# Optimization experiments

Hardware: AMD Instinct MI355X
Metric: run time of the kernel (lower is better)

Reference implementation:

```python
import jax, jax.numpy as jnp
import numpy as np

K = 9            # connections per output pixel
GA = 2           # global additional samples
RA = 2           # relative additional samples
VS = 4 + GA + RA # 2^rank neighbours + sampled
REGION = 12      # int(0.25 * 48) per spatial dim
MMULT = 0.1
MIN_SIGMA = 0.05
SIGMA_SCALE = 0.05
SIGMA_BOOST = 2.0


def setup_inputs() -> dict:
    key = jax.random.key(0)
    ks = jax.random.split(key, 8)
    b, cin, h, w = 8, 128, 48, 48
    cout = 256
    hidden = cin * 4

    def lin_init(k, fan_out, fan_in):
        bound = 1.0 / np.sqrt(fan_in)
        kw, kb = jax.random.split(k)
        W = jax.random.uniform(kw, (fan_out, fan_in), minval=-bound, maxval=bound, dtype=jnp.float32)
        bb = jax.random.uniform(kb, (fan_out,), minval=-bound, maxval=bound, dtype=jnp.float32)
        return W, bb

    x = jax.random.normal(ks[0], (b, cin, h, w), dtype=jnp.float32)
    W1, b1 = lin_init(ks[1], hidden, 2)          # toparams layer 1 (adaptive=False -> 2 coord inputs)
    W2, b2 = lin_init(ks[2], 3 * K, hidden)      # toparams layer 2 -> k means (2d) + k sigmas
    Wu, bu = lin_init(ks[3], cout, K * cin)      # unify linear
    gints = jax.random.randint(ks[4], (b, h, w, K, GA, 2), 0, h, dtype=jnp.int32)      # global samples (h==w)
    roff = jax.random.randint(ks[5], (b, h, w, K, RA, 2), 0, REGION, dtype=jnp.int32)  # relative offsets
    return {"x": x, "W1": W1, "b1": b1, "W2": W2, "b2": b2, "Wu": Wu, "bu": bu,
            "gints": gints, "roff": roff}


def reference(x, W1, b1, W2, b2, Wu, bu, gints, roff):
    b, c, h, w = x.shape
    s = jnp.array([h, w], dtype=x.dtype)                       # spatial range per dim
    s_int = jnp.array([h, w], dtype=jnp.int32)

    # normalized coordinate grid in [0,1], (h, w, 2) with [.,.,0]=row, [.,.,1]=col
    rows = jnp.arange(h, dtype=x.dtype) / (h - 1)
    cols = jnp.arange(w, dtype=x.dtype) / (w - 1)
    coords = jnp.stack(jnp.meshgrid(rows, cols, indexing='ij'), axis=-1)

    # hypernetwork: per-pixel coords -> K 2d mean offsets + K sigmas
    inp = jnp.broadcast_to(coords, (b, h, w, 2))
    hid = jax.nn.relu(inp @ W1.T + b1)
    params = hid @ W2.T + b2                                   # (b,h,w,3K)
    means_raw = params[..., :2 * K].reshape(b, h, w, K, 2)
    sig_raw = params[..., 2 * K:]                              # (b,h,w,K)

    # mids: inverse of the sigmoid scaling applied to the pixel's own coordinate
    pix = coords * (s - 1)                                     # pixel coordinates
    sc = pix / (s - 1) * 0.9999 + 0.00005
    mids = jnp.log(sc / (1.0 - sc))                            # (h,w,2)

    # transform_means: sigmoid -> [0, s-1]
    means = jax.nn.sigmoid(mids[None, :, :, None, :] + MMULT * means_raw) * (s - 1)  # (b,h,w,K,2)
    # transform_sigmas: softplus(. + boost) + min, per-dim scale, then sigma_scale
    sigmas = (jax.nn.softplus(sig_raw + SIGMA_BOOST) + MIN_SIGMA)[..., None] * s * SIGMA_SCALE  # (b,h,w,K,2)

    # ---- integer index generation (non-differentiable) ----
    fl = jnp.floor(jax.lax.stop_gradient(means)).astype(jnp.int32)   # (b,h,w,K,2)
    combos = jnp.array([[0, 0], [0, 1], [1, 0], [1, 1]], dtype=jnp.int32)
    neigh = fl[..., None, :] + combos                                 # (b,h,w,K,4,2)
    rel = fl[..., None, :] + roff - REGION // 2                       # (b,h,w,K,RA,2)
    ints = jnp.concatenate([neigh, gints, rel], axis=-2) % s_int      # (b,h,w,K,VS,2)

    # duplicate masking: zero any tuple that occurred earlier along VS
    eq = jnp.all(ints[..., :, None, :] == ints[..., None, :, :], axis=-1)  # (...,VS,VS)
    lower = jnp.tril(jnp.ones((VS, VS), dtype=bool), k=-1)
    dups = jnp.any(eq & lower, axis=-1)                               # (b,h,w,K,VS)

    # unnormalized gaussian densities of integer points under (means, sigmas)
    diff = (ints.astype(x.dtype) - means[..., None, :]) / sigmas[..., None, :]
    props = jnp.exp(-0.5 * jnp.sum(diff * diff, axis=-1))             # (b,h,w,K,VS)
    props = jnp.where(dups, jnp.zeros((), x.dtype), props)
    weights = props / jnp.sum(props, axis=-1, keepdims=True)          # mvalues are all-ones

    # irregular gather of input channel vectors at sampled pixels
    lin = ints[..., 0] * w + ints[..., 1]                             # (b,h,w,K,VS)
    flat = x.transpose(0, 2, 3, 1).reshape(b, h * w, c)
    feats = flat[jnp.arange(b)[:, None], lin.reshape(b, -1)]          # (b, h*w*K*VS, c)
    feats = feats.reshape(b, h, w, K, VS, c)

    feats = jnp.einsum('bhwkvc,bhwkv->bhwkc', feats, weights)         # weighted reduce over VS
    feats = feats.reshape(b, h, w, K * c)
    out = feats @ Wu.T + bu                                           # unify linear
    return out.transpose(0, 3, 1, 2)                                  # (b, cout, h, w)
```

## Files before the change

kernel.cpp:

```cpp
#include <hip/hip_runtime.h>
#include <hip/hip_bf16.h>

#define BB 8
#define CIN 128
#define HH 48
#define WW 48
#define HW 2304
#define KK 9
#define COUT 256
#define KC 1152
#define MM 18432
#define MT 32
#define SFP 136

typedef short bf16x8_t __attribute__((ext_vector_type(8)));
typedef float f32x16_t __attribute__((ext_vector_type(16)));
typedef float f32x4_t  __attribute__((ext_vector_type(4)));

static __device__ __forceinline__ float b2f(short u) {
    union { unsigned int i; float f; } c;
    c.i = ((unsigned int)(unsigned short)u) << 16;
    return c.f;
}

__global__ __launch_bounds__(64) void params_kernel(
    const float* __restrict__ W1, const float* __restrict__ b1,
    const float* __restrict__ W2, const float* __restrict__ b2,
    float* __restrict__ means, float* __restrict__ sigmas, int* __restrict__ fls)
{
    int p = blockIdx.x;
    int iy = p / WW, ix = p % WW;
    float ryf = (float)iy / 47.0f;
    float rxf = (float)ix / 47.0f;
    double ry = (double)ryf, rx = (double)rxf;

    __shared__ double hid[512];
    __shared__ double par[27];
    int t = threadIdx.x;

    for (int j = t; j < 512; j += 64) {
        double v = ry * (double)W1[j*2+0] + rx * (double)W1[j*2+1] + (double)b1[j];
        hid[j] = v > 0.0 ? v : 0.0;
    }
    __syncthreads();
    if (t < 27) {
        const float* w = W2 + t * 512;
        double acc = 0.0;
        for (int j = 0; j < 512; j++) acc += (double)w[j] * hid[j];
        par[t] = acc + (double)b2[t];
    }
    __syncthreads();
    if (t < KK) {
        double pixy = ry * 47.0;
        double pixx = rx * 47.0;
        double scy = pixy / 47.0 * 0.9999 + 5e-05;
        double scx = pixx / 47.0 * 0.9999 + 5e-05;
        double midy = log(scy / (1.0 - scy));
        double midx = log(scx / (1.0 - scx));
        double zy = midy + 0.1 * par[2*t+0];
        double zx = midx + 0.1 * par[2*t+1];
        double my = 47.0 / (1.0 + exp(-zy));
        double mx = 47.0 / (1.0 + exp(-zx));
        double sr = par[18 + t] + 2.0;
        double sp = (sr > 0.0 ? sr : 0.0) + log1p(exp(-fabs(sr)));
        double sg = (sp + 0.05) * 48.0 * 0.05;

        means[(p*KK + t)*2 + 0] = (float)my;
        means[(p*KK + t)*2 + 1] = (float)mx;
        sigmas[p*KK + t] = (float)sg;
        fls[(p*KK + t)*2 + 0] = (int)floor(my);
        fls[(p*KK + t)*2 + 1] = (int)floor(mx);
    }
}

__global__ __launch_bounds__(256) void transpose_kernel(
    const float* __restrict__ x, __hip_bfloat16* __restrict__ xT)
{
    __shared__ float tile[64][65];
    int b = blockIdx.z;
    int c0 = blockIdx.y * 64;
    int ij0 = blockIdx.x * 64;
    int t = threadIdx.x;
    int ijl = t & 63, cl = t >> 6;
    #pragma unroll
    for (int i = 0; i < 16; i++) {
        int cc = i*4 + cl;
        tile[cc][ijl] = x[(size_t)(b*CIN + c0 + cc) * HW + ij0 + ijl];
    }
    __syncthreads();
    int cl2 = t & 63, ijl2 = t >> 6;
    #pragma unroll
    for (int i = 0; i < 16; i++) {
        int ij = i*4 + ijl2;
        xT[(size_t)(b*HW + ij0 + ij) * CIN + c0 + cl2] = __float2bfloat16(tile[cl2][ij]);
    }
}

__global__ __launch_bounds__(256) void pack_wu(
    const float* __restrict__ Wu, bf16x8_t* __restrict__ Bp)
{
    int idx = blockIdx.x * 256 + threadIdx.x;
    int lane = idx & 63;
    int rest = idx >> 6;
    int s = rest % 72, g = rest / 72;
    int r = lane & 31, qq = lane >> 5;
    const float* src = Wu + (size_t)(g*32 + r) * KC + s*16 + qq*8;
    union { bf16x8_t v; __hip_bfloat16 h[8]; } o;
    #pragma unroll
    for (int j = 0; j < 8; j++) o.h[j] = __float2bfloat16(src[j]);
    Bp[idx] = o.v;
}

__global__ __launch_bounds__(256) void fused_kernel(
    const float* __restrict__ means, const float* __restrict__ sigmas,
    const int* __restrict__ fls, const int* __restrict__ gints,
    const int* __restrict__ roff, const short* __restrict__ xT,
    const bf16x8_t* __restrict__ Bp, const float* __restrict__ bu,
    float* __restrict__ out)
{
    __shared__ int   s_lin[KK*MT*8];
    __shared__ float s_w[KK*MT*8];
    __shared__ __align__(16) short s_feat[2][MT*SFP];

    int t = threadIdx.x;
    int m0 = blockIdx.x * MT;
    int b  = m0 / HW;
    int ij0 = m0 % HW;

    for (int p = t; p < KK*MT; p += 256) {
        int k = p >> 5, row = p & 31;
        int ij = ij0 + row;
        int bij = m0 + row;
        int fy = fls[(ij*KK + k)*2 + 0];
        int fx = fls[(ij*KK + k)*2 + 1];
        float my = means[(ij*KK + k)*2 + 0];
        float mx = means[(ij*KK + k)*2 + 1];
        float sg = sigmas[ij*KK + k];
        int lins[8]; float ws[8];
        #pragma unroll
        for (int v = 0; v < 8; v++) {
            int iy, ix;
            if (v < 4) {
                iy = fy + (v >> 1); ix = fx + (v & 1);
            } else if (v < 6) {
                int base = ((bij*KK + k)*2 + (v - 4)) * 2;
                iy = gints[base]; ix = gints[base + 1];
            } else {
                int base = ((bij*KK + k)*2 + (v - 6)) * 2;
                iy = fy + roff[base] - 6; ix = fx + roff[base + 1] - 6;
            }
            iy = ((iy % HH) + HH) % HH;
            ix = ((ix % WW) + WW) % WW;
            lins[v] = iy * WW + ix;
            float dy = ((float)iy - my) / sg;
            float dx = ((float)ix - mx) / sg;
            ws[v] = expf(-0.5f * (dy*dy + dx*dx));
        }
        #pragma unroll
        for (int v = 1; v < 8; v++) {
            bool dup = false;
            #pragma unroll
            for (int u = 0; u < 8; u++) if (u < v) dup = dup || (lins[u] == lins[v]);
            if (dup) ws[v] = 0.0f;
        }
        float sum = 0.0f;
        #pragma unroll
        for (int v = 0; v < 8; v++) sum += ws[v];
        float inv = 1.0f / sum;
        #pragma unroll
        for (int v = 0; v < 8; v++) { s_lin[p*8+v] = lins[v]; s_w[p*8+v] = ws[v] * inv; }
    }
    __syncthreads();

    const short* xb = xT + (size_t)b * (HW * CIN);
    int lane = t & 63, wave = t >> 6;
    int r = lane & 31, q = lane >> 5;
    int grow = t >> 3, gc0 = (t & 7) << 4;

    f32x16_t acc0 = {}, acc1 = {};

    for (int k = 0; k < KK; k++) {
        bf16x8_t Bf0[8], Bf1[8];
        {
            int base = ((wave*2)*72 + k*8)*64 + lane;
            #pragma unroll
            for (int si = 0; si < 8; si++) {
                Bf0[si] = Bp[base + si*64];
                Bf1[si] = Bp[base + 72*64 + si*64];
            }
        }
        {
            const int*   lp = s_lin + (k*MT + grow)*8;
            const float* wp = s_w   + (k*MT + grow)*8;
            float a0[8], a1[8];
            #pragma unroll
            for (int j = 0; j < 8; j++) { a0[j] = 0.0f; a1[j] = 0.0f; }
            #pragma unroll
            for (int v = 0; v < 8; v++) {
                int lin = lp[v];
                float w = wp[v];
                const bf16x8_t* sp = (const bf16x8_t*)(xb + (size_t)lin * CIN + gc0);
                bf16x8_t d0 = sp[0], d1 = sp[1];
                #pragma unroll
                for (int j = 0; j < 8; j++) {
                    a0[j] += w * b2f(d0[j]);
                    a1[j] += w * b2f(d1[j]);
                }
            }
            union { bf16x8_t v8; __hip_bfloat16 h[8]; } o0, o1;
            #pragma unroll
            for (int j = 0; j < 8; j++) {
                o0.h[j] = __float2bfloat16(a0[j]);
                o1.h[j] = __float2bfloat16(a1[j]);
            }
            bf16x8_t* fd = (bf16x8_t*)(&s_feat[k & 1][grow*SFP + gc0]);
            fd[0] = o0.v8;
            fd[1] = o1.v8;
        }
        __syncthreads();
        const short* fb = s_feat[k & 1];
        #pragma unroll
        for (int si = 0; si < 8; si++) {
            bf16x8_t a = *(const bf16x8_t*)(fb + r*SFP + si*16 + q*8);
            acc0 = __builtin_amdgcn_mfma_f32_32x32x16_bf16(a, Bf0[si], acc0, 0, 0, 0);
            acc1 = __builtin_amdgcn_mfma_f32_32x32x16_bf16(a, Bf1[si], acc1, 0, 0, 0);
        }
    }

    #pragma unroll
    for (int h = 0; h < 2; h++) {
        int n = wave*64 + h*32 + r;
        float bv = bu[n];
        float* oc = out + ((size_t)b * COUT + n) * HW + ij0;
        const f32x16_t a = h ? acc1 : acc0;
        #pragma unroll
        for (int g4 = 0; g4 < 4; g4++) {
            f32x4_t vv;
            vv[0] = a[g4*4+0] + bv;
            vv[1] = a[g4*4+1] + bv;
            vv[2] = a[g4*4+2] + bv;
            vv[3] = a[g4*4+3] + bv;
            *(f32x4_t*)(oc + g4*8 + q*4) = vv;
        }
    }
}

extern "C" void kernel_launch(void* const* d_in, const int* in_sizes, int n_in,
                              void* d_out, int out_size, void* d_ws, size_t ws_size,
                              hipStream_t stream)
{
    const float* x   = (const float*)d_in[0];
    const float* W1  = (const float*)d_in[1];
    const float* b1  = (const float*)d_in[2];
    const float* W2  = (const float*)d_in[3];
    const float* b2  = (const float*)d_in[4];
    const float* Wu  = (const float*)d_in[5];
    const float* bu  = (const float*)d_in[6];
    const int* gints = (const int*)d_in[7];
    const int* roff  = (const int*)d_in[8];
    float* out = (float*)d_out;

    char* ws = (char*)d_ws;
    float* ws_means  = (float*)(ws + 0);
    float* ws_sigma  = (float*)(ws + 165888);
    int*   ws_fl     = (int*  )(ws + 248832);
    short* ws_xT     = (short*)(ws + 414720);
    bf16x8_t* ws_bp  = (bf16x8_t*)(ws + 5133312);

    params_kernel<<<HW, 64, 0, stream>>>(W1, b1, W2, b2, ws_means, ws_sigma, ws_fl);
    transpose_kernel<<<dim3(HW/64, CIN/64, BB), 256, 0, stream>>>(
        x, (__hip_bfloat16*)ws_xT);
    pack_wu<<<144, 256, 0, stream>>>(Wu, ws_bp);
    fused_kernel<<<MM/MT, 256, 0, stream>>>(ws_means, ws_sigma, ws_fl, gints, roff,
                                            ws_xT, ws_bp, bu, out);
}
```

Baseline: 154.7 us.

## Merge prep kernels and software-pipeline gather with MFMA in fused kernel

The three preprocessing kernels (hypernetwork params, x transpose, Wu packing) become one launch that dispatches on block index. The params path is rewritten so each wave handles one pixel, using register-held hidden units and shuffle reductions instead of a single thread looping over 512 elements. The fused kernel moves to 512 threads, with each wave owning 32 output columns and each thread gathering 8 channels. It prefetches the next tap's gathered rows while running the previous tap's MFMAs, and packs index and weight into one int2 in shared memory. The aim is fewer launches, more parallelism in the params stage, and overlap of gather latency with matrix math, at the cost of more register pressure and a changed work split.

```diff
diff --git a/kernel.cpp b/kernel.cpp
--- a/kernel.cpp
+++ b/kernel.cpp
@@ -23,103 +23,108 @@
     return c.f;
 }
 
-__global__ __launch_bounds__(64) void params_kernel(
+__global__ __launch_bounds__(256) void prep_kernel(
+    const float* __restrict__ x, __hip_bfloat16* __restrict__ xT,
+    const float* __restrict__ Wu, bf16x8_t* __restrict__ Bp,
     const float* __restrict__ W1, const float* __restrict__ b1,
     const float* __restrict__ W2, const float* __restrict__ b2,
     float* __restrict__ means, float* __restrict__ sigmas, int* __restrict__ fls)
 {
-    int p = blockIdx.x;
-    int iy = p / WW, ix = p % WW;
-    float ryf = (float)iy / 47.0f;
-    float rxf = (float)ix / 47.0f;
-    double ry = (double)ryf, rx = (double)rxf;
-
-    __shared__ double hid[512];
-    __shared__ double par[27];
+    int bid = blockIdx.x;
     int t = threadIdx.x;
 
-    for (int j = t; j < 512; j += 64) {
-        double v = ry * (double)W1[j*2+0] + rx * (double)W1[j*2+1] + (double)b1[j];
-        hid[j] = v > 0.0 ? v : 0.0;
-    }
-    __syncthreads();
-    if (t < 27) {
-        const float* w = W2 + t * 512;
-        double acc = 0.0;
-        for (int j = 0; j < 512; j++) acc += (double)w[j] * hid[j];
-        par[t] = acc + (double)b2[t];
-    }
-    __syncthreads();
-    if (t < KK) {
-        double pixy = ry * 47.0;
-        double pixx = rx * 47.0;
-        double scy = pixy / 47.0 * 0.9999 + 5e-05;
-        double scx = pixx / 47.0 * 0.9999 + 5e-05;
-        double midy = log(scy / (1.0 - scy));
-        double midx = log(scx / (1.0 - scx));
-        double zy = midy + 0.1 * par[2*t+0];
-        double zx = midx + 0.1 * par[2*t+1];
-        double my = 47.0 / (1.0 + exp(-zy));
-        double mx = 47.0 / (1.0 + exp(-zx));
-        double sr = par[18 + t] + 2.0;
-        double sp = (sr > 0.0 ? sr : 0.0) + log1p(exp(-fabs(sr)));
-        double sg = (sp + 0.05) * 48.0 * 0.05;
-
-        means[(p*KK + t)*2 + 0] = (float)my;
-        means[(p*KK + t)*2 + 1] = (float)mx;
-        sigmas[p*KK + t] = (float)sg;
-        fls[(p*KK + t)*2 + 0] = (int)floor(my);
-        fls[(p*KK + t)*2 + 1] = (int)floor(mx);
-    }
-}
-
-__global__ __launch_bounds__(256) void transpose_kernel(
-    const float* __restrict__ x, __hip_bfloat16* __restrict__ xT)
-{
-    __shared__ float tile[64][65];
-    int b = blockIdx.z;
-    int c0 = blockIdx.y * 64;
-    int ij0 = blockIdx.x * 64;
-    int t = threadIdx.x;
-    int ijl = t & 63, cl = t >> 6;
-    #pragma unroll
-    for (int i = 0; i < 16; i++) {
-        int cc = i*4 + cl;
-        tile[cc][ijl] = x[(size_t)(b*CIN + c0 + cc) * HW + ij0 + ijl];
-    }
-    __syncthreads();
-    int cl2 = t & 63, ijl2 = t >> 6;
-    #pragma unroll
-    for (int i = 0; i < 16; i++) {
-        int ij = i*4 + ijl2;
-        xT[(size_t)(b*HW + ij0 + ij) * CIN + c0 + cl2] = __float2bfloat16(tile[cl2][ij]);
-    }
-}
-
-__global__ __launch_bounds__(256) void pack_wu(
-    const float* __restrict__ Wu, bf16x8_t* __restrict__ Bp)
-{
-    int idx = blockIdx.x * 256 + threadIdx.x;
-    int lane = idx & 63;
-    int rest = idx >> 6;
-    int s = rest % 72, g = rest / 72;
-    int r = lane & 31, qq = lane >> 5;
-    const float* src = Wu + (size_t)(g*32 + r) * KC + s*16 + qq*8;
-    union { bf16x8_t v; __hip_bfloat16 h[8]; } o;
-    #pragma unroll
-    for (int j = 0; j < 8; j++) o.h[j] = __float2bfloat16(src[j]);
-    Bp[idx] = o.v;
-}
-
-__global__ __launch_bounds__(256) void fused_kernel(
+    if (bid < 576) {
+        __shared__ float tile[64][65];
+        int ij0 = (bid % 36) * 64;
+        int c0  = ((bid / 36) % 2) * 64;
+        int b   = bid / 72;
+        int ijl = t & 63, cl = t >> 6;
+        #pragma unroll
+        for (int i = 0; i < 16; i++) {
+            int cc = i*4 + cl;
+            tile[cc][ijl] = x[(size_t)(b*CIN + c0 + cc) * HW + ij0 + ijl];
+        }
+        __syncthreads();
+        int cl2 = t & 63, ijl2 = t >> 6;
+        #pragma unroll
+        for (int i = 0; i < 16; i++) {
+            int ij = i*4 + ijl2;
+            xT[(size_t)(b*HW + ij0 + ij) * CIN + c0 + cl2] = __float2bfloat16(tile[cl2][ij]);
+        }
+    } else if (bid < 720) {
+        int idx = (bid - 576) * 256 + t;
+        int lane = idx & 63;
+        int rest = idx >> 6;
+        int s = rest % 72, g = rest / 72;
+        int r = lane & 31, qq = lane >> 5;
+        const float* src = Wu + (size_t)(g*32 + r) * KC + s*16 + qq*8;
+        union { bf16x8_t v; __hip_bfloat16 h[8]; } o;
+        #pragma unroll
+        for (int j = 0; j < 8; j++) o.h[j] = __float2bfloat16(src[j]);
+        Bp[idx] = o.v;
+    } else {
+        int wave = t >> 6, lane = t & 63;
+        int p = (bid - 720) * 4 + wave;
+        int iy = p / WW, ix = p % WW;
+        float ryf = (float)iy / 47.0f;
+        float rxf = (float)ix / 47.0f;
+        double ry = (double)ryf, rx = (double)rxf;
+
+        double h[8];
+        #pragma unroll
+        for (int jj = 0; jj < 8; jj++) {
+            int j = lane*8 + jj;
+            double v = ry * (double)W1[j*2+0] + rx * (double)W1[j*2+1] + (double)b1[j];
+            h[jj] = v > 0.0 ? v : 0.0;
+        }
+        double par[27];
+        #pragma unroll
+        for (int o = 0; o < 27; o++) {
+            const float4* w4 = (const float4*)(W2 + (size_t)o*512 + lane*8);
+            float4 wa = w4[0], wb = w4[1];
+            double s = (double)wa.x*h[0] + (double)wa.y*h[1]
+                     + (double)wa.z*h[2] + (double)wa.w*h[3]
+                     + (double)wb.x*h[4] + (double)wb.y*h[5]
+                     + (double)wb.z*h[6] + (double)wb.w*h[7];
+            par[o] = s;
+        }
+        #pragma unroll
+        for (int o = 0; o < 27; o++) {
+            #pragma unroll
+            for (int d = 1; d < 64; d <<= 1)
+                par[o] += __shfl_xor(par[o], d, 64);
+            par[o] += (double)b2[o];
+        }
+        if (lane < KK) {
+            int k = lane;
+            double scy = ry * 0.9999 + 5e-05;
+            double scx = rx * 0.9999 + 5e-05;
+            double midy = log(scy / (1.0 - scy));
+            double midx = log(scx / (1.0 - scx));
+            double zy = midy + 0.1 * par[2*k+0];
+            double zx = midx + 0.1 * par[2*k+1];
+            double my = 47.0 / (1.0 + exp(-zy));
+            double mx = 47.0 / (1.0 + exp(-zx));
+            double sr = par[18 + k] + 2.0;
+            double sp = (sr > 0.0 ? sr : 0.0) + log1p(exp(-fabs(sr)));
+            double sg = (sp + 0.05) * 48.0 * 0.05;
+            means[(p*KK + k)*2 + 0] = (float)my;
+            means[(p*KK + k)*2 + 1] = (float)mx;
+            sigmas[p*KK + k] = (float)sg;
+            fls[(p*KK + k)*2 + 0] = (int)floor(my);
+            fls[(p*KK + k)*2 + 1] = (int)floor(mx);
+        }
+    }
+}
+
+__global__ __launch_bounds__(512, 4) void fused_kernel(
     const float* __restrict__ means, const float* __restrict__ sigmas,
     const int* __restrict__ fls, const int* __restrict__ gints,
     const int* __restrict__ roff, const short* __restrict__ xT,
     const bf16x8_t* __restrict__ Bp, const float* __restrict__ bu,
     float* __restrict__ out)
 {
-    __shared__ int   s_lin[KK*MT*8];
-    __shared__ float s_w[KK*MT*8];
+    __shared__ int2 s_tap[KK*MT*8];
     __shared__ __align__(16) short s_feat[2][MT*SFP];
 
     int t = threadIdx.x;
@@ -127,7 +132,8 @@
     int b  = m0 / HW;
     int ij0 = m0 % HW;
 
-    for (int p = t; p < KK*MT; p += 256) {
+    if (t < KK*MT) {
+        int p = t;
         int k = p >> 5, row = p & 31;
         int ij = ij0 + row;
         int bij = m0 + row;
@@ -168,80 +174,83 @@
         for (int v = 0; v < 8; v++) sum += ws[v];
         float inv = 1.0f / sum;
         #pragma unroll
-        for (int v = 0; v < 8; v++) { s_lin[p*8+v] = lins[v]; s_w[p*8+v] = ws[v] * inv; }
+        for (int v = 0; v < 8; v++)
+            s_tap[p*8+v] = make_int2(lins[v], __float_as_int(ws[v] * inv));
     }
     __syncthreads();
 
     const short* xb = xT + (size_t)b * (HW * CIN);
     int lane = t & 63, wave = t >> 6;
     int r = lane & 31, q = lane >> 5;
-    int grow = t >> 3, gc0 = (t & 7) << 4;
-
-    f32x16_t acc0 = {}, acc1 = {};
-
+    int grow = t >> 4, gc0 = (t & 15) << 3;
+
+    f32x16_t acc = {};
+    bf16x8_t Bf[8];
+    bf16x8_t tap[8];
+    float    wgt[8];
+
+    #pragma unroll
     for (int k = 0; k < KK; k++) {
-        bf16x8_t Bf0[8], Bf1[8];
         {
-            int base = ((wave*2)*72 + k*8)*64 + lane;
+            const int2* tp = &s_tap[(k*MT + grow)*8];
+            #pragma unroll
+            for (int v = 0; v < 8; v++) {
+                int2 e = tp[v];
+                wgt[v] = __int_as_float(e.y);
+                tap[v] = *(const bf16x8_t*)(xb + (size_t)e.x * CIN + gc0);
+            }
+        }
+        if (k > 0) {
+            const short* fb = s_feat[(k-1) & 1];
             #pragma unroll
             for (int si = 0; si < 8; si++) {
-                Bf0[si] = Bp[base + si*64];
-                Bf1[si] = Bp[base + 72*64 + si*64];
+                bf16x8_t a = *(const bf16x8_t*)(fb + r*SFP + si*16 + q*8);
+                acc = __builtin_amdgcn_mfma_f32_32x32x16_bf16(a, Bf[si], acc, 0, 0, 0);
             }
         }
         {
-            const int*   lp = s_lin + (k*MT + grow)*8;
-            const float* wp = s_w   + (k*MT + grow)*8;
-            float a0[8], a1[8];
-            #pragma unroll
-            for (int j = 0; j < 8; j++) { a0[j] = 0.0f; a1[j] = 0.0f; }
+            int base = (wave*72 + k*8)*64 + lane;
+            #pragma unroll
+            for (int si = 0; si < 8; si++) Bf[si] = Bp[base + si*64];
+        }
+        {
+            float a0[8];
+            #pragma unroll
+            for (int j = 0; j < 8; j++) a0[j] = 0.0f;
             #pragma unroll
             for (int v = 0; v < 8; v++) {
-                int lin = lp[v];
-                float w = wp[v];
-                const bf16x8_t* sp = (const bf16x8_t*)(xb + (size_t)lin * CIN + gc0);
-                bf16x8_t d0 = sp[0], d1 = sp[1];
+                float w = wgt[v];
+                bf16x8_t d8 = tap[v];
                 #pragma unroll
-                for (int j = 0; j < 8; j++) {
-                    a0[j] += w * b2f(d0[j]);
-                    a1[j] += w * b2f(d1[j]);
-                }
-            }
-            union { bf16x8_t v8; __hip_bfloat16 h[8]; } o0, o1;
-            #pragma unroll
-            for (int j = 0; j < 8; j++) {
-                o0.h[j] = __float2bfloat16(a0[j]);
-                o1.h[j] = __float2bfloat16(a1[j]);
-            }
-            bf16x8_t* fd = (bf16x8_t*)(&s_feat[k & 1][grow*SFP + gc0]);
-            fd[0] = o0.v8;
-            fd[1] = o1.v8;
+                for (int j = 0; j < 8; j++) a0[j] += w * b2f(d8[j]);
+            }
+            union { bf16x8_t v8; __hip_bfloat16 hh[8]; } o;
+            #pragma unroll
+            for (int j = 0; j < 8; j++) o.hh[j] = __float2bfloat16(a0[j]);
+            *(bf16x8_t*)(&s_feat[k & 1][grow*SFP + gc0]) = o.v8;
         }
         __syncthreads();
-        const short* fb = s_feat[k & 1];
+    }
+    {
+        const short* fb = s_feat[(KK-1) & 1];
         #pragma unroll
         for (int si = 0; si < 8; si++) {
             bf16x8_t a = *(const bf16x8_t*)(fb + r*SFP + si*16 + q*8);
-            acc0 = __builtin_amdgcn_mfma_f32_32x32x16_bf16(a, Bf0[si], acc0, 0, 0, 0);
-            acc1 = __builtin_amdgcn_mfma_f32_32x32x16_bf16(a, Bf1[si], acc1, 0, 0, 0);
-        }
-    }
-
+            acc = __builtin_amdgcn_mfma_f32_32x32x16_bf16(a, Bf[si], acc, 0, 0, 0);
+        }
+    }
+
+    int n = wave*32 + r;
+    float bv = bu[n];
+    float* oc = out + ((size_t)b * COUT + n) * HW + ij0;
     #pragma unroll
-    for (int h = 0; h < 2; h++) {
-        int n = wave*64 + h*32 + r;
-        float bv = bu[n];
-        float* oc = out + ((size_t)b * COUT + n) * HW + ij0;
-        const f32x16_t a = h ? acc1 : acc0;
-        #pragma unroll
-        for (int g4 = 0; g4 < 4; g4++) {
-            f32x4_t vv;
-            vv[0] = a[g4*4+0] + bv;
-            vv[1] = a[g4*4+1] + bv;
-            vv[2] = a[g4*4+2] + bv;
-            vv[3] = a[g4*4+3] + bv;
-            *(f32x4_t*)(oc + g4*8 + q*4) = vv;
-        }
+    for (int g4 = 0; g4 < 4; g4++) {
+        f32x4_t vv;
+        vv[0] = acc[g4*4+0] + bv;
+        vv[1] = acc[g4*4+1] + bv;
+        vv[2] = acc[g4*4+2] + bv;
+        vv[3] = acc[g4*4+3] + bv;
+        *(f32x4_t*)(oc + g4*8 + q*4) = vv;
     }
 }
 
@@ -267,10 +276,9 @@
     short* ws_xT     = (short*)(ws + 414720);
     bf16x8_t* ws_bp  = (bf16x8_t*)(ws + 5133312);
 
-    params_kernel<<<HW, 64, 0, stream>>>(W1, b1, W2, b2, ws_means, ws_sigma, ws_fl);
-    transpose_kernel<<<dim3(HW/64, CIN/64, BB), 256, 0, stream>>>(
-        x, (__hip_bfloat16*)ws_xT);
-    pack_wu<<<144, 256, 0, stream>>>(Wu, ws_bp);
-    fused_kernel<<<MM/MT, 256, 0, stream>>>(ws_means, ws_sigma, ws_fl, gints, roff,
+    prep_kernel<<<1296, 256, 0, stream>>>(x, (__hip_bfloat16*)ws_xT, Wu, ws_bp,
+                                          W1, b1, W2, b2,
+                                          ws_means, ws_sigma, ws_fl);
+    fused_kernel<<<MM/MT, 512, 0, stream>>>(ws_means, ws_sigma, ws_fl, gints, roff,
                                             ws_xT, ws_bp, bu, out);
 }
```

Measured after the change: 146.1 us. 1.06x faster.
